# Kernel optimization log

Hardware: AMD Instinct MI355X
Metric: run time of the kernel (lower is better)

Reference implementation:

```python
import jax
import jax.numpy as jnp
import numpy as np

# Module configuration (matches init_kwargs)
N, C, H, W = 8, 256, 64, 64
CO, KH, KW = 256, 3, 3
SH, SW = 1, 1
PH, PW = 1, 1
DH, DW = 1, 1
G, DG = 1, 1
K = KH * KW
HO = (H + 2 * PH - (DH * (KH - 1) + 1)) // SH + 1
WO = (W + 2 * PW - (DW * (KW - 1) + 1)) // SW + 1


def setup_inputs() -> dict:
    key = jax.random.key(0)
    k1, k2, k3, k4 = jax.random.split(key, 4)
    x = jax.random.normal(k1, (N, C, H, W), dtype=jnp.float32)
    offset = jax.random.normal(k2, (N, DG * 2 * K, HO, WO), dtype=jnp.float32)
    mask = jax.random.uniform(k3, (N, DG * K, HO, WO), dtype=jnp.float32)
    stdv = 1.0 / np.sqrt(C * KH * KW)
    weight = jax.random.uniform(k4, (CO, C // G, KH, KW), dtype=jnp.float32,
                                minval=-stdv, maxval=stdv)
    return {"x": x, "offset": offset, "mask": mask, "weight": weight}


def _deform_sample(x, offset, mask):
    """Modulated deformable bilinear sampling (DCNv2 im2col).

    Returns columns [N, C, K, HO, WO].
    """
    Cg = C // DG
    # offset layout: [N, DG, K, 2(y,x), HO, WO]
    off = offset.reshape(N, DG, K, 2, HO, WO)
    off_y, off_x = off[:, :, :, 0], off[:, :, :, 1]

    # Base sampling grid per kernel tap: [K, HO, WO] broadcastable
    kgy = (jnp.repeat(jnp.arange(KH), KW) * DH).astype(jnp.float32)  # [K]
    kgx = (jnp.tile(jnp.arange(KW), KH) * DW).astype(jnp.float32)    # [K]
    oy = (jnp.arange(HO) * SH - PH).astype(jnp.float32)              # [HO]
    ox = (jnp.arange(WO) * SW - PW).astype(jnp.float32)              # [WO]
    py = kgy[:, None, None] + oy[None, :, None] + off_y  # [N,DG,K,HO,WO]
    px = kgx[:, None, None] + ox[None, None, :] + off_x  # [N,DG,K,HO,WO]

    y0 = jnp.floor(py)
    x0 = jnp.floor(px)
    ly = py - y0
    lx = px - x0
    y0i = y0.astype(jnp.int32)
    x0i = x0.astype(jnp.int32)
    y1i = y0i + 1
    x1i = x0i + 1

    xf = x.reshape(N, DG, Cg, H * W)

    def gather_one(xf_nd, idx_nd):
        # xf_nd: [Cg, H*W], idx_nd: [K*HO*WO] -> [Cg, K*HO*WO]
        return xf_nd[:, idx_nd]

    gather = jax.vmap(jax.vmap(gather_one))  # over N, DG

    def corner(yi, xi, wgt):
        valid = (yi >= 0) & (yi < H) & (xi >= 0) & (xi < W)
        yc = jnp.clip(yi, 0, H - 1)
        xc = jnp.clip(xi, 0, W - 1)
        idx = (yc * W + xc).reshape(N, DG, K * HO * WO)
        g = gather(xf, idx).reshape(N, DG, Cg, K, HO, WO)
        w = (wgt * valid.astype(x.dtype))[:, :, None]  # [N,DG,1,K,HO,WO]
        return g * w

    cols = corner(y0i, x0i, (1.0 - ly) * (1.0 - lx))
    cols = cols + corner(y0i, x1i, (1.0 - ly) * lx)
    cols = cols + corner(y1i, x0i, ly * (1.0 - lx))
    cols = cols + corner(y1i, x1i, ly * lx)

    # modulation
    m = mask.reshape(N, DG, 1, K, HO, WO)
    cols = cols * m
    return cols.reshape(N, C, K, HO, WO)


def reference(x, offset, mask, weight):
    cols = _deform_sample(x, offset, mask)              # [N,C,K,HO,WO]
    colsg = cols.reshape(N, G, C // G, K, HO, WO)
    wg = weight.reshape(G, CO // G, C // G, K)
    out = jnp.einsum('ngckhw,gock->ngohw', colsg, wg)
    return out.reshape(N, CO, HO, WO)
```

## Files before the change

### kernel.cpp

```cpp
#include <hip/hip_runtime.h>
#include <hip/hip_bf16.h>
#include <hip/hip_fp16.h>
#include <stdint.h>

#define N_   8
#define C_   256
#define H_   64
#define W_   64
#define CO_  256
#define K_   9
#define HO_  64
#define WO_  64
#define CK_  (C_ * K_)
#define P_   (HO_ * WO_)

#define BN   64
#define BK   64
#define NT   36
#define NTHR 512

typedef __attribute__((ext_vector_type(8))) _Float16 f16x8;
typedef __attribute__((ext_vector_type(4))) float f32x4;

__device__ __forceinline__ unsigned short f2bf(float f) {
    uint32_t u = __builtin_bit_cast(uint32_t, f);
    uint32_t r = (u + 0x7FFFu + ((u >> 16) & 1u)) >> 16;
    return (unsigned short)r;
}
__device__ __forceinline__ float bf2f(unsigned short u) {
    return __builtin_bit_cast(float, (uint32_t)u << 16);
}
__device__ __forceinline__ unsigned short f2h(float f) {
    return __builtin_bit_cast(unsigned short, (_Float16)f);
}


__global__ __launch_bounds__(256)
void transpose_x(const float* __restrict__ x, unsigned short* __restrict__ xT) {
    __shared__ float t[64][65];
    const int n  = blockIdx.z;
    const int c0 = blockIdx.y * 64;
    const int h0 = blockIdx.x * 64;
    const int tx = threadIdx.x & 63;
    const int ty = threadIdx.x >> 6;
    const float* xp = x + ((size_t)n * C_ + c0) * P_ + h0;
    #pragma unroll
    for (int i = 0; i < 16; ++i) {
        int c = ty * 16 + i;
        t[c][tx] = xp[(size_t)c * P_ + tx];
    }
    __syncthreads();
    unsigned short* op = xT + ((size_t)n * P_ + h0) * C_ + c0;
    #pragma unroll
    for (int i = 0; i < 16; ++i) {
        int hw = ty * 16 + i;
        op[(size_t)hw * C_ + tx] = f2h(t[tx][hw]);
    }
}

__global__ __launch_bounds__(256)
void reorder_w(const float* __restrict__ w, unsigned short* __restrict__ Wt) {
    const int co = blockIdx.x;
    const int c  = threadIdx.x;
    const float* src = w + (size_t)co * CK_ + (size_t)c * K_;
    float v[9];
    #pragma unroll
    for (int k = 0; k < 9; ++k) v[k] = src[k];
    #pragma unroll
    for (int k = 0; k < 9; ++k)
        Wt[(size_t)co * CK_ + k * C_ + c] = f2h(v[k]);
}

__device__ __forceinline__ void barrier_lgkm_only() {
    __builtin_amdgcn_sched_barrier(0);
    asm volatile("s_waitcnt lgkmcnt(0)" ::: "memory");
    __builtin_amdgcn_s_barrier();
    __builtin_amdgcn_sched_barrier(0);
}

__global__ __launch_bounds__(NTHR, 4)
void dcn_main(const unsigned short* __restrict__ xT,
              const unsigned short* __restrict__ Wt,
              const float* __restrict__ offset,
              const float* __restrict__ mask,
              float* __restrict__ out) {
    __shared__ uint2 sIdx[BN * K_];
    __shared__ uint4 sWd [BN * K_];
    __shared__ unsigned short sWs[CO_ * BK];
    __shared__ unsigned short sBs[BN * BK];

    const int tid = threadIdx.x;
    const int bid = blockIdx.x;
    const int n   = bid & 7;
    const int p0  = (bid >> 3) * BN;

    for (int e = tid; e < BN * K_; e += NTHR) {
        int pl = e / K_;
        int k  = e - pl * K_;
        int p  = p0 + pl;
        int ho = p >> 6, wo = p & 63;
        float offy = offset[(size_t)((n * 2 * K_ + 2 * k)     * P_) + p];
        float offx = offset[(size_t)((n * 2 * K_ + 2 * k + 1) * P_) + p];
        float m    = mask  [(size_t)((n * K_ + k) * P_) + p];
        float py = (float)(k / 3 + ho - 1) + offy;
        float px = (float)(k % 3 + wo - 1) + offx;
        float y0f = floorf(py), x0f = floorf(px);
        float ly = py - y0f,   lx = px - x0f;
        int y0 = (int)y0f, x0 = (int)x0f;
        int y1 = y0 + 1,   x1 = x0 + 1;
        bool vy0 = (y0 >= 0) & (y0 < H_);
        bool vy1 = (y1 >= 0) & (y1 < H_);
        bool vx0 = (x0 >= 0) & (x0 < W_);
        bool vx1 = (x1 >= 0) & (x1 < W_);
        float w00 = (1.f - ly) * (1.f - lx) * m * ((vy0 & vx0) ? 1.f : 0.f);
        float w01 = (1.f - ly) * lx         * m * ((vy0 & vx1) ? 1.f : 0.f);
        float w10 = ly * (1.f - lx)         * m * ((vy1 & vx0) ? 1.f : 0.f);
        float w11 = ly * lx                 * m * ((vy1 & vx1) ? 1.f : 0.f);
        unsigned int cy0 = (unsigned)min(max(y0, 0), H_ - 1);
        unsigned int cy1 = (unsigned)min(max(y1, 0), H_ - 1);
        unsigned int cx0 = (unsigned)min(max(x0, 0), W_ - 1);
        unsigned int cx1 = (unsigned)min(max(x1, 0), W_ - 1);
        sIdx[e] = make_uint2((cy0 * W_ + cx0) | ((cy0 * W_ + cx1) << 16),
                             (cy1 * W_ + cx0) | ((cy1 * W_ + cx1) << 16));
        sWd[e] = make_uint4((unsigned)f2h(w00) * 0x10001u,
                            (unsigned)f2h(w01) * 0x10001u,
                            (unsigned)f2h(w10) * 0x10001u,
                            (unsigned)f2h(w11) * 0x10001u);
    }
    __syncthreads();

    const unsigned short* xTn = xT + (size_t)n * P_ * C_;

    const int spl = tid >> 3;
    const int cs8 = (tid & 7) * 8;
    char* bdst = (char*)sBs + spl * 128 + (((tid & 7) ^ (spl & 7)) << 4);
    const int wco  = tid >> 1;
    const int wchq = (tid & 1) * 4;
    const int wswz = wco & 7;
    char* wrow = (char*)sWs + wco * 128;
    const unsigned short* wsrcbase = Wt + (size_t)wco * CK_ + (tid & 1) * 32;

    const int lane = tid & 63;
    const int wid  = tid >> 6;
    const int wm   = (wid & 3) * 64;
    const int wp   = (wid >> 2) * 32;
    const int l15  = lane & 15;
    const int l4   = lane >> 4;
    const int slA  = l4 ^ (l15 & 7);

    f32x4 acc[4][2] = {};

    uint4 qa, qb, qc, qd;
    uint4 wq0, wq1, wq2, wq3;

    {
        const unsigned short* ws = wsrcbase;
        wq0 = *(const uint4*)(ws);
        wq1 = *(const uint4*)(ws + 8);
        wq2 = *(const uint4*)(ws + 16);
        wq3 = *(const uint4*)(ws + 24);
        uint2 id = sIdx[spl * K_];
        const unsigned short* base = xTn + cs8;
        qa = *(const uint4*)(base + ((size_t)(id.x & 0xFFFFu) << 8));
        qb = *(const uint4*)(base + ((size_t)(id.x >> 16)     << 8));
        qc = *(const uint4*)(base + ((size_t)(id.y & 0xFFFFu) << 8));
        qd = *(const uint4*)(base + ((size_t)(id.y >> 16)     << 8));
    }

    for (int t = 0; t < NT; ++t) {
        const int k = t >> 2;

        barrier_lgkm_only();

        asm volatile("s_waitcnt vmcnt(0)" ::: "memory");

        {
            *(uint4*)(wrow + (((wchq + 0) ^ wswz) << 4)) = wq0;
            *(uint4*)(wrow + (((wchq + 1) ^ wswz) << 4)) = wq1;
            *(uint4*)(wrow + (((wchq + 2) ^ wswz) << 4)) = wq2;
            *(uint4*)(wrow + (((wchq + 3) ^ wswz) << 4)) = wq3;

            uint4 wv = sWd[spl * K_ + k];
            __half2 W0 = __builtin_bit_cast(__half2, wv.x);
            __half2 W1 = __builtin_bit_cast(__half2, wv.y);
            __half2 W2 = __builtin_bit_cast(__half2, wv.z);
            __half2 W3 = __builtin_bit_cast(__half2, wv.w);
            const unsigned* pa = (const unsigned*)&qa;
            const unsigned* pb = (const unsigned*)&qb;
            const unsigned* pc = (const unsigned*)&qc;
            const unsigned* pd = (const unsigned*)&qd;
            unsigned rr[4];
            #pragma unroll
            for (int h = 0; h < 4; ++h) {
                __half2 v = __hmul2(W0, __builtin_bit_cast(__half2, pa[h]));
                v = __hfma2(W1, __builtin_bit_cast(__half2, pb[h]), v);
                v = __hfma2(W2, __builtin_bit_cast(__half2, pc[h]), v);
                v = __hfma2(W3, __builtin_bit_cast(__half2, pd[h]), v);
                rr[h] = __builtin_bit_cast(unsigned, v);
            }
            *(uint4*)bdst = make_uint4(rr[0], rr[1], rr[2], rr[3]);
        }

        if (t + 1 < NT) {
            const int kn  = (t + 1) >> 2;
            const int c0n = ((t + 1) & 3) * 64;
            const unsigned short* ws = wsrcbase + kn * C_ + c0n;
            wq0 = *(const uint4*)(ws);
            wq1 = *(const uint4*)(ws + 8);
            wq2 = *(const uint4*)(ws + 16);
            wq3 = *(const uint4*)(ws + 24);
            uint2 id = sIdx[spl * K_ + kn];
            const unsigned short* base = xTn + c0n + cs8;
            qa = *(const uint4*)(base + ((size_t)(id.x & 0xFFFFu) << 8));
            qb = *(const uint4*)(base + ((size_t)(id.x >> 16)     << 8));
            qc = *(const uint4*)(base + ((size_t)(id.y & 0xFFFFu) << 8));
            qd = *(const uint4*)(base + ((size_t)(id.y >> 16)     << 8));
        }

        barrier_lgkm_only();

        #pragma unroll
        for (int ks = 0; ks < 2; ++ks) {
            const int sl = slA ^ (ks << 2);
            f16x8 b0 = *(const f16x8*)((const char*)sBs + (wp      + l15) * 128 + (sl << 4));
            f16x8 b1 = *(const f16x8*)((const char*)sBs + (wp + 16 + l15) * 128 + (sl << 4));
            #pragma unroll
            for (int m = 0; m < 4; ++m) {
                f16x8 a = *(const f16x8*)((const char*)sWs + (wm + m * 16 + l15) * 128 + (sl << 4));
                acc[m][0] = __builtin_amdgcn_mfma_f32_16x16x32_f16(a, b0, acc[m][0], 0, 0, 0);
                acc[m][1] = __builtin_amdgcn_mfma_f32_16x16x32_f16(a, b1, acc[m][1], 0, 0, 0);
            }
        }
    }

    float* outn = out + (size_t)n * CO_ * P_;
    #pragma unroll
    for (int m = 0; m < 4; ++m) {
        int co = wm + m * 16 + l4 * 4;
        #pragma unroll
        for (int nn = 0; nn < 2; ++nn) {
            int p = p0 + wp + nn * 16 + l15;
            #pragma unroll
            for (int r = 0; r < 4; ++r) {
                outn[(size_t)(co + r) * P_ + p] = acc[m][nn][r];
            }
        }
    }
}

template <int TAG>
__global__ __launch_bounds__(512, 2)
void dcn_fb(const float* __restrict__ x,
            const float* __restrict__ offset,
            const float* __restrict__ mask,
            const float* __restrict__ weight,
            float* __restrict__ out) {
    typedef __attribute__((ext_vector_type(8))) short bf16x8;
    __shared__ uint2  sIdx[128 * K_];
    __shared__ float4 sW  [128 * K_];
    __shared__ unsigned short sWs[CO_ * 32];
    __shared__ unsigned short sBs[128 * 32];

    const int tid = threadIdx.x;
    const int n  = blockIdx.y;
    const int p0 = blockIdx.x * 128;

    for (int e = tid; e < 128 * K_; e += 512) {
        int pl = e / K_;
        int k  = e - pl * K_;
        int p  = p0 + pl;
        int ho = p >> 6, wo = p & 63;
        float offy = offset[(size_t)((n * 2 * K_ + 2 * k)     * P_) + p];
        float offx = offset[(size_t)((n * 2 * K_ + 2 * k + 1) * P_) + p];
        float m    = mask  [(size_t)((n * K_ + k) * P_) + p];
        float py = (float)(k / 3 + ho - 1) + offy;
        float px = (float)(k % 3 + wo - 1) + offx;
        float y0f = floorf(py), x0f = floorf(px);
        float ly = py - y0f,   lx = px - x0f;
        int y0 = (int)y0f, x0 = (int)x0f;
        int y1 = y0 + 1,   x1 = x0 + 1;
        bool vy0 = (y0 >= 0) & (y0 < H_);
        bool vy1 = (y1 >= 0) & (y1 < H_);
        bool vx0 = (x0 >= 0) & (x0 < W_);
        bool vx1 = (x1 >= 0) & (x1 < W_);
        float w00 = (1.f - ly) * (1.f - lx) * m * ((vy0 & vx0) ? 1.f : 0.f);
        float w01 = (1.f - ly) * lx         * m * ((vy0 & vx1) ? 1.f : 0.f);
        float w10 = ly * (1.f - lx)         * m * ((vy1 & vx0) ? 1.f : 0.f);
        float w11 = ly * lx                 * m * ((vy1 & vx1) ? 1.f : 0.f);
        unsigned int cy0 = (unsigned)min(max(y0, 0), H_ - 1);
        unsigned int cy1 = (unsigned)min(max(y1, 0), H_ - 1);
        unsigned int cx0 = (unsigned)min(max(x0, 0), W_ - 1);
        unsigned int cx1 = (unsigned)min(max(x1, 0), W_ - 1);
        sIdx[e] = make_uint2((cy0 * W_ + cx0) | ((cy0 * W_ + cx1) << 16),
                             (cy1 * W_ + cx0) | ((cy1 * W_ + cx1) << 16));
        sW[e]   = make_float4(w00, w01, w10, w11);
    }

    const float* xn = x + (size_t)n * C_ * P_;
    const int pl   = tid >> 2;
    const int pl9  = pl * K_;
    const int ckb  = (tid & 3) * 8;
    const int wco  = tid >> 1;
    const int wck  = (tid & 1) * 16;

    const int lane = tid & 63;
    const int wid  = tid >> 6;
    const int wm   = (wid & 1) * 128;
    const int wp   = (wid >> 1) * 32;
    const int l15  = lane & 15;
    const int l4   = lane >> 4;

    f32x4 acc[8][2] = {};

    for (int ck0 = 0; ck0 < CK_; ck0 += 32) {
        __syncthreads();
        {
            const float4* wsrc = (const float4*)(weight + (size_t)wco * CK_ + ck0 + wck);
            float4 wa = wsrc[0], wb = wsrc[1], wc = wsrc[2], wd = wsrc[3];
            uint4 q0, q1;
            q0.x = f2bf(wa.x) | ((unsigned)f2bf(wa.y) << 16);
            q0.y = f2bf(wa.z) | ((unsigned)f2bf(wa.w) << 16);
            q0.z = f2bf(wb.x) | ((unsigned)f2bf(wb.y) << 16);
            q0.w = f2bf(wb.z) | ((unsigned)f2bf(wb.w) << 16);
            q1.x = f2bf(wc.x) | ((unsigned)f2bf(wc.y) << 16);
            q1.y = f2bf(wc.z) | ((unsigned)f2bf(wc.w) << 16);
            q1.z = f2bf(wd.x) | ((unsigned)f2bf(wd.y) << 16);
            q1.w = f2bf(wd.z) | ((unsigned)f2bf(wd.w) << 16);
            *(uint4*)&sWs[wco * 32 + wck]     = q0;
            *(uint4*)&sWs[wco * 32 + wck + 8] = q1;
        }
        {
            int ckstart = ck0 + ckb;
            int cc = ckstart / 9;
            int kk = ckstart - cc * 9;
            unsigned int packed[4];
            unsigned short colv[8];
            #pragma unroll
            for (int j = 0; j < 8; ++j) {
                int e = pl9 + kk;
                uint2  id = sIdx[e];
                float4 wv = sW[e];
                const float* xp = xn + ((size_t)cc << 12);
                float v = wv.x * xp[id.x & 0xFFFFu]
                        + wv.y * xp[id.x >> 16]
                        + wv.z * xp[id.y & 0xFFFFu]
                        + wv.w * xp[id.y >> 16];
                colv[j] = f2bf(v);
                ++kk; if (kk == 9) { kk = 0; ++cc; }
            }
            packed[0] = colv[0] | ((unsigned)colv[1] << 16);
            packed[1] = colv[2] | ((unsigned)colv[3] << 16);
            packed[2] = colv[4] | ((unsigned)colv[5] << 16);
            packed[3] = colv[6] | ((unsigned)colv[7] << 16);
            *(uint4*)&sBs[pl * 32 + ckb] = *(uint4*)packed;
        }
        __syncthreads();
        bf16x8 bfr0 = *(const bf16x8*)&sBs[(wp + l15)      * 32 + l4 * 8];
        bf16x8 bfr1 = *(const bf16x8*)&sBs[(wp + 16 + l15) * 32 + l4 * 8];
        #pragma unroll
        for (int m = 0; m < 8; ++m) {
            bf16x8 afr = *(const bf16x8*)&sWs[(wm + m * 16 + l15) * 32 + l4 * 8];
            acc[m][0] = __builtin_amdgcn_mfma_f32_16x16x32_bf16(afr, bfr0, acc[m][0], 0, 0, 0);
            acc[m][1] = __builtin_amdgcn_mfma_f32_16x16x32_bf16(afr, bfr1, acc[m][1], 0, 0, 0);
        }
    }

    float* outn = out + (size_t)n * CO_ * P_;
    #pragma unroll
    for (int m = 0; m < 8; ++m) {
        int co = wm + m * 16 + l4 * 4;
        #pragma unroll
        for (int nn = 0; nn < 2; ++nn) {
            int p = p0 + wp + nn * 16 + l15;
            #pragma unroll
            for (int r = 0; r < 4; ++r) {
                outn[(size_t)(co + r) * P_ + p] = acc[m][nn][r];
            }
        }
    }
}

extern "C" void kernel_launch(void* const* d_in, const int* in_sizes, int n_in,
                              void* d_out, int out_size, void* d_ws, size_t ws_size,
                              hipStream_t stream) {
    const float* x      = (const float*)d_in[0];
    const float* offset = (const float*)d_in[1];
    const float* mask   = (const float*)d_in[2];
    const float* weight = (const float*)d_in[3];
    float* out = (float*)d_out;

    const size_t xT_elems = (size_t)N_ * P_ * C_;
    const size_t Wt_elems = (size_t)CO_ * CK_;
    const size_t need     = (xT_elems + Wt_elems) * sizeof(unsigned short);

    if (ws_size >= need) {
        unsigned short* xT = (unsigned short*)d_ws;
        unsigned short* Wt = xT + xT_elems;
        transpose_x<<<dim3(P_ / 64, C_ / 64, N_), dim3(256), 0, stream>>>(x, xT);
        reorder_w<<<dim3(CO_), dim3(256), 0, stream>>>(weight, Wt);
        dcn_main<<<dim3((P_ / BN) * N_), dim3(NTHR), 0, stream>>>(xT, Wt, offset, mask, out);
    } else if (ws_size >= (8u << 20)) {
        dcn_fb<1><<<dim3(P_ / 128, N_), dim3(512), 0, stream>>>(x, offset, mask, weight, out);
    } else {
        dcn_fb<0><<<dim3(P_ / 128, N_), dim3(512), 0, stream>>>(x, offset, mask, weight, out);
    }
}
```

Measured before the change: 84.86 us.

## Double pixel tile per block to 128 and widen per-thread sampling work

Raises the pixel tile from 64 to 128, so each block's 256-output-channel weight slice staged in LDS is reused across twice as many pixels. Each thread now gathers and blends 16 channels instead of 8, and each wave computes a 64x64 output tile with a 4x4 MFMA accumulator array. This halves the block count and the total weight traffic per output, at the cost of more registers and LDS, with launch bounds lowered from 4 to 2 blocks per CU. The grid launch must match the new block count.

```diff
diff --git a/kernel.cpp b/kernel.cpp
--- a/kernel.cpp
+++ b/kernel.cpp
@@ -14,7 +14,7 @@
 #define CK_  (C_ * K_)
 #define P_   (HO_ * WO_)
 
-#define BN   64
+#define BN   128
 #define BK   64
 #define NT   36
 #define NTHR 512
@@ -78,7 +78,14 @@
     __builtin_amdgcn_sched_barrier(0);
 }
 
-__global__ __launch_bounds__(NTHR, 4)
+#define COMB(dst, A, B, Cc, D) do {                                   \
+    __half2 _v = __hmul2(W0, __builtin_bit_cast(__half2, (A)));       \
+    _v = __hfma2(W1, __builtin_bit_cast(__half2, (B)), _v);           \
+    _v = __hfma2(W2, __builtin_bit_cast(__half2, (Cc)), _v);          \
+    _v = __hfma2(W3, __builtin_bit_cast(__half2, (D)), _v);           \
+    (dst) = __builtin_bit_cast(unsigned, _v); } while (0)
+
+__global__ __launch_bounds__(NTHR, 2)
 void dcn_main(const unsigned short* __restrict__ xT,
               const unsigned short* __restrict__ Wt,
               const float* __restrict__ offset,
@@ -131,9 +138,11 @@
 
     const unsigned short* xTn = xT + (size_t)n * P_ * C_;
 
-    const int spl = tid >> 3;
-    const int cs8 = (tid & 7) * 8;
-    char* bdst = (char*)sBs + spl * 128 + (((tid & 7) ^ (spl & 7)) << 4);
+    const int spl  = tid >> 2;
+    const int cs16 = (tid & 3) * 16;
+    const int bsw  = spl & 7;
+    char* bdst0 = (char*)sBs + spl * 128 + ((((tid & 3) * 2)     ^ bsw) << 4);
+    char* bdst1 = (char*)sBs + spl * 128 + ((((tid & 3) * 2 + 1) ^ bsw) << 4);
     const int wco  = tid >> 1;
     const int wchq = (tid & 1) * 4;
     const int wswz = wco & 7;
@@ -143,14 +152,14 @@
     const int lane = tid & 63;
     const int wid  = tid >> 6;
     const int wm   = (wid & 3) * 64;
-    const int wp   = (wid >> 2) * 32;
+    const int wp   = (wid >> 2) * 64;
     const int l15  = lane & 15;
     const int l4   = lane >> 4;
     const int slA  = l4 ^ (l15 & 7);
 
-    f32x4 acc[4][2] = {};
-
-    uint4 qa, qb, qc, qd;
+    f32x4 acc[4][4] = {};
+
+    uint4 qa0, qa1, qb0, qb1, qc0, qc1, qd0, qd1;
     uint4 wq0, wq1, wq2, wq3;
 
     {
@@ -160,11 +169,15 @@
         wq2 = *(const uint4*)(ws + 16);
         wq3 = *(const uint4*)(ws + 24);
         uint2 id = sIdx[spl * K_];
-        const unsigned short* base = xTn + cs8;
-        qa = *(const uint4*)(base + ((size_t)(id.x & 0xFFFFu) << 8));
-        qb = *(const uint4*)(base + ((size_t)(id.x >> 16)     << 8));
-        qc = *(const uint4*)(base + ((size_t)(id.y & 0xFFFFu) << 8));
-        qd = *(const uint4*)(base + ((size_t)(id.y >> 16)     << 8));
+        const unsigned short* base = xTn + cs16;
+        const unsigned short* ba = base + ((size_t)(id.x & 0xFFFFu) << 8);
+        const unsigned short* bb = base + ((size_t)(id.x >> 16)     << 8);
+        const unsigned short* bc = base + ((size_t)(id.y & 0xFFFFu) << 8);
+        const unsigned short* bd = base + ((size_t)(id.y >> 16)     << 8);
+        qa0 = *(const uint4*)(ba); qa1 = *(const uint4*)(ba + 8);
+        qb0 = *(const uint4*)(bb); qb1 = *(const uint4*)(bb + 8);
+        qc0 = *(const uint4*)(bc); qc1 = *(const uint4*)(bc + 8);
+        qd0 = *(const uint4*)(bd); qd1 = *(const uint4*)(bd + 8);
     }
 
     for (int t = 0; t < NT; ++t) {
@@ -185,20 +198,17 @@
             __half2 W1 = __builtin_bit_cast(__half2, wv.y);
             __half2 W2 = __builtin_bit_cast(__half2, wv.z);
             __half2 W3 = __builtin_bit_cast(__half2, wv.w);
-            const unsigned* pa = (const unsigned*)&qa;
-            const unsigned* pb = (const unsigned*)&qb;
-            const unsigned* pc = (const unsigned*)&qc;
-            const unsigned* pd = (const unsigned*)&qd;
-            unsigned rr[4];
-            #pragma unroll
-            for (int h = 0; h < 4; ++h) {
-                __half2 v = __hmul2(W0, __builtin_bit_cast(__half2, pa[h]));
-                v = __hfma2(W1, __builtin_bit_cast(__half2, pb[h]), v);
-                v = __hfma2(W2, __builtin_bit_cast(__half2, pc[h]), v);
-                v = __hfma2(W3, __builtin_bit_cast(__half2, pd[h]), v);
-                rr[h] = __builtin_bit_cast(unsigned, v);
-            }
-            *(uint4*)bdst = make_uint4(rr[0], rr[1], rr[2], rr[3]);
+            uint4 r0, r1;
+            COMB(r0.x, qa0.x, qb0.x, qc0.x, qd0.x);
+            COMB(r0.y, qa0.y, qb0.y, qc0.y, qd0.y);
+            COMB(r0.z, qa0.z, qb0.z, qc0.z, qd0.z);
+            COMB(r0.w, qa0.w, qb0.w, qc0.w, qd0.w);
+            COMB(r1.x, qa1.x, qb1.x, qc1.x, qd1.x);
+            COMB(r1.y, qa1.y, qb1.y, qc1.y, qd1.y);
+            COMB(r1.z, qa1.z, qb1.z, qc1.z, qd1.z);
+            COMB(r1.w, qa1.w, qb1.w, qc1.w, qd1.w);
+            *(uint4*)bdst0 = r0;
+            *(uint4*)bdst1 = r1;
         }
 
         if (t + 1 < NT) {
@@ -210,11 +220,15 @@
             wq2 = *(const uint4*)(ws + 16);
             wq3 = *(const uint4*)(ws + 24);
             uint2 id = sIdx[spl * K_ + kn];
-            const unsigned short* base = xTn + c0n + cs8;
-            qa = *(const uint4*)(base + ((size_t)(id.x & 0xFFFFu) << 8));
-            qb = *(const uint4*)(base + ((size_t)(id.x >> 16)     << 8));
-            qc = *(const uint4*)(base + ((size_t)(id.y & 0xFFFFu) << 8));
-            qd = *(const uint4*)(base + ((size_t)(id.y >> 16)     << 8));
+            const unsigned short* base = xTn + c0n + cs16;
+            const unsigned short* ba = base + ((size_t)(id.x & 0xFFFFu) << 8);
+            const unsigned short* bb = base + ((size_t)(id.x >> 16)     << 8);
+            const unsigned short* bc = base + ((size_t)(id.y & 0xFFFFu) << 8);
+            const unsigned short* bd = base + ((size_t)(id.y >> 16)     << 8);
+            qa0 = *(const uint4*)(ba); qa1 = *(const uint4*)(ba + 8);
+            qb0 = *(const uint4*)(bb); qb1 = *(const uint4*)(bb + 8);
+            qc0 = *(const uint4*)(bc); qc1 = *(const uint4*)(bc + 8);
+            qd0 = *(const uint4*)(bd); qd1 = *(const uint4*)(bd + 8);
         }
 
         barrier_lgkm_only();
@@ -224,11 +238,15 @@
             const int sl = slA ^ (ks << 2);
             f16x8 b0 = *(const f16x8*)((const char*)sBs + (wp      + l15) * 128 + (sl << 4));
             f16x8 b1 = *(const f16x8*)((const char*)sBs + (wp + 16 + l15) * 128 + (sl << 4));
+            f16x8 b2 = *(const f16x8*)((const char*)sBs + (wp + 32 + l15) * 128 + (sl << 4));
+            f16x8 b3 = *(const f16x8*)((const char*)sBs + (wp + 48 + l15) * 128 + (sl << 4));
             #pragma unroll
             for (int m = 0; m < 4; ++m) {
                 f16x8 a = *(const f16x8*)((const char*)sWs + (wm + m * 16 + l15) * 128 + (sl << 4));
                 acc[m][0] = __builtin_amdgcn_mfma_f32_16x16x32_f16(a, b0, acc[m][0], 0, 0, 0);
                 acc[m][1] = __builtin_amdgcn_mfma_f32_16x16x32_f16(a, b1, acc[m][1], 0, 0, 0);
+                acc[m][2] = __builtin_amdgcn_mfma_f32_16x16x32_f16(a, b2, acc[m][2], 0, 0, 0);
+                acc[m][3] = __builtin_amdgcn_mfma_f32_16x16x32_f16(a, b3, acc[m][3], 0, 0, 0);
             }
         }
     }
@@ -238,7 +256,7 @@
     for (int m = 0; m < 4; ++m) {
         int co = wm + m * 16 + l4 * 4;
         #pragma unroll
-        for (int nn = 0; nn < 2; ++nn) {
+        for (int nn = 0; nn < 4; ++nn) {
             int p = p0 + wp + nn * 16 + l15;
             #pragma unroll
             for (int r = 0; r < 4; ++r) {
```

New measurement: 83.87 us. No clear change (-1.2%).
